# Performance work log

Measured on AMD Instinct MI355X. Metric: run time of the kernel, lower is better.

Reference implementation:

```python
import jax, jax.numpy as jnp
import numpy as np

N = 50000       # n_nodes
E = 800000      # n_edges
DIN = 64
DH = 64
DOUT = 64


def setup_inputs() -> dict:
    key = jax.random.key(0)
    k0, k1, k2, k3, k4 = jax.random.split(key, 5)
    x = jax.random.normal(k0, (N, DIN), dtype=jnp.float32)
    edge_index = jax.random.randint(k1, (2, E), 0, N, dtype=jnp.int32)
    # learnable per-edge weight (nn.Parameter); positive init keeps gcn_norm well-defined
    edge_weight = jax.random.uniform(k2, (E,), jnp.float32, 0.1, 1.0)
    W1 = jax.random.normal(k3, (DH, DIN), dtype=jnp.float32) * (1.0 / np.sqrt(DIN))
    b1 = jnp.zeros((DH,), jnp.float32)
    W2 = jax.random.normal(k4, (DOUT, DH), dtype=jnp.float32) * (1.0 / np.sqrt(DH))
    b2 = jnp.zeros((DOUT,), jnp.float32)
    return {"x": x, "edge_weight": edge_weight, "W1": W1, "b1": b1,
            "W2": W2, "b2": b2, "edge_index": edge_index}


def _gcn_norm(edge_index, edge_weight, n):
    # PyG gcn_norm: add self-loops (weight 1), symmetric normalization.
    loop = jnp.arange(n, dtype=edge_index.dtype)
    row = jnp.concatenate([edge_index[0], loop])   # source nodes
    col = jnp.concatenate([edge_index[1], loop])   # target nodes
    w = jnp.concatenate([edge_weight, jnp.ones((n,), edge_weight.dtype)])
    deg = jax.ops.segment_sum(w, col, num_segments=n)
    dinv = jnp.where(deg > 0, jax.lax.rsqrt(jnp.where(deg > 0, deg, 1.0)), 0.0)
    norm = dinv[row] * w * dinv[col]               # [E + N]
    return row, col, norm


def _gcn_layer(x, W, b, row, col, norm, n):
    h = x @ W.T                                     # [N, out]
    # gather source features, scale by norm, scatter-add into targets
    out = jax.ops.segment_sum(h[row] * norm[:, None], col, num_segments=n)
    return out + b


def reference(x, edge_weight, W1, b1, W2, b2, edge_index):
    n = x.shape[0]
    row, col, norm = _gcn_norm(edge_index, edge_weight, n)
    h = _gcn_layer(x, W1, b1, row, col, norm, n)
    h = jax.nn.relu(h)                              # self.pre: ReLU + Dropout (identity in eval)
    return _gcn_layer(h, W2, b2, row, col, norm, n)
```

## Files before the change

kernel.cpp:

```cpp
#include <hip/hip_runtime.h>

#define D 64
#define GN 128
#define SW 68
#define SX 132
#define MAXDEG 64
#define RBITS_C 8
#define RANGE_C 256
#define MAXB_C 5120
#define RANGE_F 64
#define APB 2048

typedef unsigned long long u64;
typedef unsigned int u32;
typedef unsigned short u16;
typedef unsigned char u8;

__device__ __forceinline__ float4 fma4(float4 w, float s, float4 c) {
    c.x = fmaf(w.x, s, c.x); c.y = fmaf(w.y, s, c.y);
    c.z = fmaf(w.z, s, c.z); c.w = fmaf(w.w, s, c.w);
    return c;
}

__device__ __forceinline__ u32 f2bf(float f) {
    u32 u = __float_as_uint(f);
    return (u + 0x7FFFu + ((u >> 16) & 1u)) >> 16;
}
__device__ __forceinline__ u32 pack2(float a, float b) { return f2bf(a) | (f2bf(b) << 16); }
__device__ __forceinline__ float blo(u32 u) { return __uint_as_float(u << 16); }
__device__ __forceinline__ float bhi(u32 u) { return __uint_as_float(u & 0xFFFF0000u); }

__global__ __launch_bounds__(256) void k_bucket(
        const int* __restrict__ ei, const float* __restrict__ ew,
        u64* __restrict__ barr, u32* __restrict__ gcount, int E, int NB) {
    __shared__ u64 srec[APB];
    __shared__ u8  sbkt[APB];
    __shared__ u32 scnt[256];
    __shared__ u32 sbase[256];

    int t = threadIdx.x;
    int e0 = blockIdx.x * APB;
    int ne = min(APB, E - e0);

    for (int i = t; i < 256; i += 256) scnt[i] = 0;
    __syncthreads();

    for (int i = t; i < ne; i += 256) {
        int e   = e0 + i;
        int r   = ei[e];
        int c   = ei[(size_t)E + e];
        float w = ew[e];
        int b   = c >> RBITS_C;
        srec[i] = ((u64)__float_as_uint(w) << 32)
                | (u32)r | ((u32)(c & (RANGE_C - 1)) << 20);
        sbkt[i] = (u8)b;
        atomicAdd(&scnt[b], 1u);
    }
    __syncthreads();

    for (int i = t; i < NB; i += 256) {
        u32 cnt = scnt[i];
        sbase[i] = cnt ? atomicAdd(&gcount[i], cnt) : 0u;
        scnt[i] = 0;
    }
    __syncthreads();

    for (int i = t; i < ne; i += 256) {
        int b   = sbkt[i];
        u32 rk  = atomicAdd(&scnt[b], 1u);
        u32 pos = sbase[b] + rk;
        if (pos < MAXB_C) barr[(size_t)b * MAXB_C + pos] = srec[i];
    }
}

__global__ __launch_bounds__(256) void k_csr(
        const u64* __restrict__ barr, const u32* __restrict__ gcount,
        u64* __restrict__ degcnt, int2* __restrict__ eg, int N) {
    __shared__ __align__(16) int2 seg[RANGE_F * MAXDEG];
    __shared__ u32   scnt[RANGE_F];
    __shared__ float sdeg[RANGE_F];

    int fb = blockIdx.x;
    int cb = fb >> 2;
    int sub = fb & 3;
    int t = threadIdx.x;
    u32 cnt = min(gcount[cb], (u32)MAXB_C);
    int base_c = fb << 6;

    if (t < RANGE_F) { scnt[t] = 0; sdeg[t] = 1.0f; }
    __syncthreads();

    const u64* bp = barr + (size_t)cb * MAXB_C;
    for (u32 i = t; i < cnt; i += 256) {
        u64 rec = bp[i];
        int cl8 = (int)((rec >> 20) & 0xFFu);
        if ((cl8 >> 6) != sub) continue;
        int cl  = cl8 & (RANGE_F - 1);
        int src = (int)(rec & 0xFFFFFu);
        u32 wb  = (u32)(rec >> 32);
        u32 rank = atomicAdd(&scnt[cl], 1u);
        atomicAdd(&sdeg[cl], __uint_as_float(wb));
        if (rank < MAXDEG) seg[(cl << 6) + rank] = make_int2(src, (int)wb);
    }
    __syncthreads();

    if (t < RANGE_F) {
        int n = base_c + t;
        if (n < N) {
            u32 c2 = min(scnt[t], (u32)MAXDEG);
            float dd = rsqrtf(sdeg[t]);
            degcnt[n] = ((u64)c2 << 32) | (u64)__float_as_uint(dd);
        }
    }

    int nt = min(RANGE_F, N - base_c);
    const int4* s4 = (const int4*)seg;
    int4* d4 = (int4*)(eg + ((size_t)base_c << 6));
    int tot = nt << 5;
    for (int i = t; i < tot; i += 256) {
        int cl = i >> 5;
        int lv = (int)min(scnt[cl], (u32)MAXDEG);
        if (((i & 31) << 1) < lv) d4[i] = s4[i];
    }
}

__global__ __launch_bounds__(256) void k_fold(
        const u64* __restrict__ degcnt, int2* __restrict__ eg, int N, int nwaves) {
    int lane = threadIdx.x & 63;
    int w0 = blockIdx.x * 4 + (threadIdx.x >> 6);
    const u32* dv = (const u32*)degcnt;

    for (int n = w0; n < N; n += nwaves) {
        u64 dcn = degcnt[n];
        int c = min((int)(dcn >> 32), MAXDEG);
        float dinv_n = __uint_as_float((u32)dcn);
        if (lane < c) {
            size_t s = ((size_t)n << 6) + lane;
            int2 ee = eg[s];
            float di = __uint_as_float(dv[(size_t)ee.x << 1]);
            float wf = __int_as_float(ee.y) * di * dinv_n;
            eg[s] = make_int2(ee.x, __float_as_int(wf));
        }
    }
}

__global__ __launch_bounds__(256) void k_gemm(
        const float* __restrict__ in, const float* __restrict__ W,
        u16* __restrict__ h, int N) {
    __shared__ __align__(16) float sWt[D * SW];
    __shared__ __align__(16) float sxT[D * SX];

    int t = threadIdx.x;
    int node0 = blockIdx.x * GN;

    for (int i = t; i < D * D / 4; i += 256) {
        int j = i >> 4, k4 = i & 15;
        float4 w = ((const float4*)W)[i];
        sWt[(4 * k4 + 0) * SW + j] = w.x;
        sWt[(4 * k4 + 1) * SW + j] = w.y;
        sWt[(4 * k4 + 2) * SW + j] = w.z;
        sWt[(4 * k4 + 3) * SW + j] = w.w;
    }
    for (int i = t; i < GN * D / 4; i += 256) {
        int nn = i >> 4, k4 = i & 15;
        int n = node0 + nn;
        float4 v = make_float4(0.f, 0.f, 0.f, 0.f);
        if (n < N) v = ((const float4*)(in + (size_t)n * D))[k4];
        sxT[(4 * k4 + 0) * SX + nn] = v.x;
        sxT[(4 * k4 + 1) * SX + nn] = v.y;
        sxT[(4 * k4 + 2) * SX + nn] = v.z;
        sxT[(4 * k4 + 3) * SX + nn] = v.w;
    }
    __syncthreads();

    int jg = (t & 7) * 8;
    int ng = (t >> 3) * 4;
    float4 a0[4], a1[4];
    #pragma unroll
    for (int a = 0; a < 4; ++a) {
        a0[a] = make_float4(0.f, 0.f, 0.f, 0.f);
        a1[a] = make_float4(0.f, 0.f, 0.f, 0.f);
    }

    #pragma unroll 8
    for (int k = 0; k < D; ++k) {
        const float* wr = &sWt[k * SW + jg];
        float4 w0 = *(const float4*)wr;
        float4 w1 = *(const float4*)(wr + 4);
        float4 xv = *(const float4*)&sxT[k * SX + ng];
        a0[0] = fma4(w0, xv.x, a0[0]);  a1[0] = fma4(w1, xv.x, a1[0]);
        a0[1] = fma4(w0, xv.y, a0[1]);  a1[1] = fma4(w1, xv.y, a1[1]);
        a0[2] = fma4(w0, xv.z, a0[2]);  a1[2] = fma4(w1, xv.z, a1[2]);
        a0[3] = fma4(w0, xv.w, a0[3]);  a1[3] = fma4(w1, xv.w, a1[3]);
    }

    #pragma unroll
    for (int a = 0; a < 4; ++a) {
        int n = node0 + ng + a;
        if (n >= N) continue;
        uint4 st;
        st.x = pack2(a0[a].x, a0[a].y);
        st.y = pack2(a0[a].z, a0[a].w);
        st.z = pack2(a1[a].x, a1[a].y);
        st.w = pack2(a1[a].z, a1[a].w);
        *(uint4*)(h + (size_t)n * D + jg) = st;
    }
}

__device__ __forceinline__ void gather8(
        const u16* __restrict__ h, const u64* __restrict__ degcnt,
        const int2* __restrict__ eg, float4 bia, float4 bib,
        u64* __restrict__ se,
        int n, int lane, float acc[8]) {
    int g = lane >> 3;
    int f = (lane & 7) * 8;
    u64 dcn = degcnt[n];
    int c = min((int)(dcn >> 32), MAXDEG);
    float dinv_n = __uint_as_float((u32)dcn);

    size_t s = (size_t)n << 6;
    if (lane < c) {
        int2 ee = eg[s + lane];
        se[lane] = ((u64)(u32)ee.y << 32) | (u32)ee.x;
    }

    #pragma unroll
    for (int i = 0; i < 8; ++i) acc[i] = 0.f;

    if (g == 0) {
        float d2 = dinv_n * dinv_n;
        uint4 hv = *(const uint4*)(h + ((size_t)n << 6) + f);
        acc[0] = fmaf(blo(hv.x), d2, bia.x); acc[1] = fmaf(bhi(hv.x), d2, bia.y);
        acc[2] = fmaf(blo(hv.y), d2, bia.z); acc[3] = fmaf(bhi(hv.y), d2, bia.w);
        acc[4] = fmaf(blo(hv.z), d2, bib.x); acc[5] = fmaf(bhi(hv.z), d2, bib.y);
        acc[6] = fmaf(blo(hv.w), d2, bib.z); acc[7] = fmaf(bhi(hv.w), d2, bib.w);
    }

    #pragma unroll
    for (int k = 0; k < 8; ++k) {
        int e = g + (k << 3);
        if (e < c) {
            u64 rec = se[e];
            int src = (int)(u32)rec;
            float w = __uint_as_float((u32)(rec >> 32));
            uint4 hv = *(const uint4*)(h + ((size_t)src << 6) + f);
            acc[0] = fmaf(blo(hv.x), w, acc[0]); acc[1] = fmaf(bhi(hv.x), w, acc[1]);
            acc[2] = fmaf(blo(hv.y), w, acc[2]); acc[3] = fmaf(bhi(hv.y), w, acc[3]);
            acc[4] = fmaf(blo(hv.z), w, acc[4]); acc[5] = fmaf(bhi(hv.z), w, acc[5]);
            acc[6] = fmaf(blo(hv.w), w, acc[6]); acc[7] = fmaf(bhi(hv.w), w, acc[7]);
        }
    }
}

__global__ __launch_bounds__(512) void k_agg_g2(
        const u16* __restrict__ h, const u64* __restrict__ degcnt,
        const int2* __restrict__ eg, const float* __restrict__ b1,
        const float* __restrict__ W2, u16* __restrict__ h2, int N) {
    __shared__ __align__(16) float4 sA[8 * 64];
    __shared__ __align__(16) float4 sB[8 * 64];
    __shared__ u64 sedge[8][64];

    int t = threadIdx.x;
    {
        int jj = t >> 6, l = t & 63;
        int gg = l >> 3, kk = l & 7;
        const float4* w4 = (const float4*)(W2 + ((size_t)(gg * 8 + jj) << 6) + kk * 8);
        sA[t] = w4[0];
        sB[t] = w4[1];
    }
    __syncthreads();

    int wid = t >> 6, lane = t & 63;
    int n = blockIdx.x * 8 + wid;
    if (n >= N) return;
    int g = lane >> 3, f = (lane & 7) * 8;

    float4 bia = *(const float4*)(b1 + f);
    float4 bib = *(const float4*)(b1 + f + 4);

    float acc[8];
    gather8(h, degcnt, eg, bia, bib, sedge[wid], n, lane, acc);

    #pragma unroll
    for (int k = 0; k < 8; ++k) {
        acc[k] += __shfl_xor(acc[k], 8);
        acc[k] += __shfl_xor(acc[k], 16);
        acc[k] += __shfl_xor(acc[k], 32);
    }

    float r[8];
    #pragma unroll
    for (int k = 0; k < 8; ++k) r[k] = fmaxf(acc[k], 0.f);

    float p[8];
    #pragma unroll
    for (int jj = 0; jj < 8; ++jj) {
        float4 wa = sA[(jj << 6) + lane];
        float4 wb = sB[(jj << 6) + lane];
        float v;
        v = r[0] * wa.x;         v = fmaf(r[1], wa.y, v);
        v = fmaf(r[2], wa.z, v); v = fmaf(r[3], wa.w, v);
        v = fmaf(r[4], wb.x, v); v = fmaf(r[5], wb.y, v);
        v = fmaf(r[6], wb.z, v); v = fmaf(r[7], wb.w, v);
        p[jj] = v;
    }
    #pragma unroll
    for (int jj = 0; jj < 8; ++jj) {
        p[jj] += __shfl_xor(p[jj], 1);
        p[jj] += __shfl_xor(p[jj], 2);
        p[jj] += __shfl_xor(p[jj], 4);
    }

    if ((lane & 7) == 0) {
        uint4 st;
        st.x = pack2(p[0], p[1]);
        st.y = pack2(p[2], p[3]);
        st.z = pack2(p[4], p[5]);
        st.w = pack2(p[6], p[7]);
        *(uint4*)(h2 + ((size_t)n << 6) + g * 8) = st;
    }
}

__global__ __launch_bounds__(256) void k_aggregate(
        const u16* __restrict__ h, const u64* __restrict__ degcnt,
        const int2* __restrict__ eg, const float* __restrict__ b,
        float* __restrict__ out, int N) {
    __shared__ u64 sedge[4][64];

    int t = threadIdx.x, wid = t >> 6, lane = t & 63;
    int n = blockIdx.x * 4 + wid;
    if (n >= N) return;
    int g = lane >> 3, f = (lane & 7) * 8;

    float4 bia = *(const float4*)(b + f);
    float4 bib = *(const float4*)(b + f + 4);

    float acc[8];
    gather8(h, degcnt, eg, bia, bib, sedge[wid], n, lane, acc);

    #pragma unroll
    for (int k = 0; k < 8; ++k) {
        acc[k] += __shfl_xor(acc[k], 8);
        acc[k] += __shfl_xor(acc[k], 16);
        acc[k] += __shfl_xor(acc[k], 32);
    }

    if (g == 0) {
        float4* o = (float4*)(out + ((size_t)n << 6) + f);
        o[0] = make_float4(acc[0], acc[1], acc[2], acc[3]);
        o[1] = make_float4(acc[4], acc[5], acc[6], acc[7]);
    }
}

extern "C" void kernel_launch(void* const* d_in, const int* in_sizes, int n_in,
                              void* d_out, int out_size, void* d_ws, size_t ws_size,
                              hipStream_t stream) {
    const float* x  = (const float*)d_in[0];
    const float* ew = (const float*)d_in[1];
    const float* W1 = (const float*)d_in[2];
    const float* b1 = (const float*)d_in[3];
    const float* W2 = (const float*)d_in[4];
    const float* b2 = (const float*)d_in[5];
    const int*   ei = (const int*)d_in[6];

    int N = in_sizes[0] / D;
    int E = in_sizes[1];
    int NBC = (N + RANGE_C - 1) >> RBITS_C;
    int NBF = (N + RANGE_F - 1) / RANGE_F;
    float* out = (float*)d_out;

    char* p = (char*)d_ws;
    u64*   degcnt = (u64*)p;   p += (size_t)N * 8;
    int2*  eg     = (int2*)p;  p += (size_t)N * MAXDEG * 8;
    u16*   h      = (u16*)p;   p += (size_t)N * D * 2;
    u16*   h2     = (u16*)p;   p += (size_t)N * D * 2;
    u64*   barr   = (u64*)p;   p += (size_t)NBC * MAXB_C * 8;
    u32*   gcount = (u32*)p;   p += 4096;

    dim3 blk(256);
    int gemm_grid   = (N + GN - 1) / GN;
    int bucket_grid = (E + APB - 1) / APB;
    int fold_grid   = 3125;
    int aggf_grid   = (N + 7) / 8;
    int agg_grid    = (N + 3) / 4;

    hipMemsetAsync(gcount, 0, 4096, stream);

    k_bucket<<<dim3(bucket_grid), blk, 0, stream>>>(ei, ew, barr, gcount, E, NBC);
    k_csr<<<dim3(NBF), blk, 0, stream>>>(barr, gcount, degcnt, eg, N);
    k_fold<<<dim3(fold_grid), blk, 0, stream>>>(degcnt, eg, N, fold_grid * 4);

    k_gemm<<<dim3(gemm_grid), blk, 0, stream>>>(x, W1, h, N);

    k_agg_g2<<<dim3(aggf_grid), dim3(512), 0, stream>>>(h, degcnt, eg, b1, W2, h2, N);

    k_aggregate<<<dim3(agg_grid), blk, 0, stream>>>(h2, degcnt, eg, b2, out, N);
}
```

Measured before the change: 193.4 us.

## Fuse edge-weight normalization into first aggregation and use one-feature-per-lane gathers

```diff
diff --git a/kernel.cpp b/kernel.cpp
--- a/kernel.cpp
+++ b/kernel.cpp
@@ -27,8 +27,7 @@
     return (u + 0x7FFFu + ((u >> 16) & 1u)) >> 16;
 }
 __device__ __forceinline__ u32 pack2(float a, float b) { return f2bf(a) | (f2bf(b) << 16); }
-__device__ __forceinline__ float blo(u32 u) { return __uint_as_float(u << 16); }
-__device__ __forceinline__ float bhi(u32 u) { return __uint_as_float(u & 0xFFFF0000u); }
+__device__ __forceinline__ float bf2f(u32 hv) { return __uint_as_float(hv << 16); }
 
 __global__ __launch_bounds__(256) void k_bucket(
         const int* __restrict__ ei, const float* __restrict__ ew,
@@ -124,26 +123,6 @@
     }
 }
 
-__global__ __launch_bounds__(256) void k_fold(
-        const u64* __restrict__ degcnt, int2* __restrict__ eg, int N, int nwaves) {
-    int lane = threadIdx.x & 63;
-    int w0 = blockIdx.x * 4 + (threadIdx.x >> 6);
-    const u32* dv = (const u32*)degcnt;
-
-    for (int n = w0; n < N; n += nwaves) {
-        u64 dcn = degcnt[n];
-        int c = min((int)(dcn >> 32), MAXDEG);
-        float dinv_n = __uint_as_float((u32)dcn);
-        if (lane < c) {
-            size_t s = ((size_t)n << 6) + lane;
-            int2 ee = eg[s];
-            float di = __uint_as_float(dv[(size_t)ee.x << 1]);
-            float wf = __int_as_float(ee.y) * di * dinv_n;
-            eg[s] = make_int2(ee.x, __float_as_int(wf));
-        }
-    }
-}
-
 __global__ __launch_bounds__(256) void k_gemm(
         const float* __restrict__ in, const float* __restrict__ W,
         u16* __restrict__ h, int N) {
@@ -207,58 +186,14 @@
     }
 }
 
-__device__ __forceinline__ void gather8(
-        const u16* __restrict__ h, const u64* __restrict__ degcnt,
-        const int2* __restrict__ eg, float4 bia, float4 bib,
-        u64* __restrict__ se,
-        int n, int lane, float acc[8]) {
-    int g = lane >> 3;
-    int f = (lane & 7) * 8;
-    u64 dcn = degcnt[n];
-    int c = min((int)(dcn >> 32), MAXDEG);
-    float dinv_n = __uint_as_float((u32)dcn);
-
-    size_t s = (size_t)n << 6;
-    if (lane < c) {
-        int2 ee = eg[s + lane];
-        se[lane] = ((u64)(u32)ee.y << 32) | (u32)ee.x;
-    }
-
-    #pragma unroll
-    for (int i = 0; i < 8; ++i) acc[i] = 0.f;
-
-    if (g == 0) {
-        float d2 = dinv_n * dinv_n;
-        uint4 hv = *(const uint4*)(h + ((size_t)n << 6) + f);
-        acc[0] = fmaf(blo(hv.x), d2, bia.x); acc[1] = fmaf(bhi(hv.x), d2, bia.y);
-        acc[2] = fmaf(blo(hv.y), d2, bia.z); acc[3] = fmaf(bhi(hv.y), d2, bia.w);
-        acc[4] = fmaf(blo(hv.z), d2, bib.x); acc[5] = fmaf(bhi(hv.z), d2, bib.y);
-        acc[6] = fmaf(blo(hv.w), d2, bib.z); acc[7] = fmaf(bhi(hv.w), d2, bib.w);
-    }
-
-    #pragma unroll
-    for (int k = 0; k < 8; ++k) {
-        int e = g + (k << 3);
-        if (e < c) {
-            u64 rec = se[e];
-            int src = (int)(u32)rec;
-            float w = __uint_as_float((u32)(rec >> 32));
-            uint4 hv = *(const uint4*)(h + ((size_t)src << 6) + f);
-            acc[0] = fmaf(blo(hv.x), w, acc[0]); acc[1] = fmaf(bhi(hv.x), w, acc[1]);
-            acc[2] = fmaf(blo(hv.y), w, acc[2]); acc[3] = fmaf(bhi(hv.y), w, acc[3]);
-            acc[4] = fmaf(blo(hv.z), w, acc[4]); acc[5] = fmaf(bhi(hv.z), w, acc[5]);
-            acc[6] = fmaf(blo(hv.w), w, acc[6]); acc[7] = fmaf(bhi(hv.w), w, acc[7]);
-        }
-    }
-}
-
 __global__ __launch_bounds__(512) void k_agg_g2(
         const u16* __restrict__ h, const u64* __restrict__ degcnt,
-        const int2* __restrict__ eg, const float* __restrict__ b1,
+        int2* __restrict__ eg, const float* __restrict__ b1,
         const float* __restrict__ W2, u16* __restrict__ h2, int N) {
     __shared__ __align__(16) float4 sA[8 * 64];
     __shared__ __align__(16) float4 sB[8 * 64];
     __shared__ u64 sedge[8][64];
+    __shared__ __align__(16) float srow[8][64];
 
     int t = threadIdx.x;
     {
@@ -273,24 +208,41 @@
     int wid = t >> 6, lane = t & 63;
     int n = blockIdx.x * 8 + wid;
     if (n >= N) return;
-    int g = lane >> 3, f = (lane & 7) * 8;
-
-    float4 bia = *(const float4*)(b1 + f);
-    float4 bib = *(const float4*)(b1 + f + 4);
-
-    float acc[8];
-    gather8(h, degcnt, eg, bia, bib, sedge[wid], n, lane, acc);
-
-    #pragma unroll
-    for (int k = 0; k < 8; ++k) {
-        acc[k] += __shfl_xor(acc[k], 8);
-        acc[k] += __shfl_xor(acc[k], 16);
-        acc[k] += __shfl_xor(acc[k], 32);
-    }
-
-    float r[8];
-    #pragma unroll
-    for (int k = 0; k < 8; ++k) r[k] = fmaxf(acc[k], 0.f);
+
+    const u32* dv = (const u32*)degcnt;
+    u64 dcn = degcnt[n];
+    int c = min((int)(dcn >> 32), MAXDEG);
+    float dinv_n = __uint_as_float((u32)dcn);
+    u64* se = sedge[wid];
+    size_t s = (size_t)n << 6;
+
+    if (lane < c) {
+        int2 ee = eg[s + lane];
+        float di = __uint_as_float(dv[(size_t)ee.x << 1]);
+        float wf = __int_as_float(ee.y) * di * dinv_n;
+        eg[s + lane] = make_int2(ee.x, __float_as_int(wf));
+        se[lane] = ((u64)__float_as_uint(wf) << 32) | (u32)ee.x;
+    }
+
+    float acc = b1[lane];
+    acc = fmaf(bf2f(h[s + lane]), dinv_n * dinv_n, acc);
+
+    #pragma unroll
+    for (int e = 0; e < MAXDEG; ++e) {
+        if (e < c) {
+            u64 rec = se[e];
+            u32 src = (u32)rec;
+            float wf = __uint_as_float((u32)(rec >> 32));
+            acc = fmaf(bf2f(h[((size_t)src << 6) + lane]), wf, acc);
+        }
+    }
+
+    float r = fmaxf(acc, 0.f);
+    srow[wid][lane] = r;
+
+    int g = lane >> 3, kb = (lane & 7) * 8;
+    float4 ra = *(const float4*)&srow[wid][kb];
+    float4 rb = *(const float4*)&srow[wid][kb + 4];
 
     float p[8];
     #pragma unroll
@@ -298,10 +250,10 @@
         float4 wa = sA[(jj << 6) + lane];
         float4 wb = sB[(jj << 6) + lane];
         float v;
-        v = r[0] * wa.x;         v = fmaf(r[1], wa.y, v);
-        v = fmaf(r[2], wa.z, v); v = fmaf(r[3], wa.w, v);
-        v = fmaf(r[4], wb.x, v); v = fmaf(r[5], wb.y, v);
-        v = fmaf(r[6], wb.z, v); v = fmaf(r[7], wb.w, v);
+        v = ra.x * wa.x;         v = fmaf(ra.y, wa.y, v);
+        v = fmaf(ra.z, wa.z, v); v = fmaf(ra.w, wa.w, v);
+        v = fmaf(rb.x, wb.x, v); v = fmaf(rb.y, wb.y, v);
+        v = fmaf(rb.z, wb.z, v); v = fmaf(rb.w, wb.w, v);
         p[jj] = v;
     }
     #pragma unroll
@@ -317,7 +269,7 @@
         st.y = pack2(p[2], p[3]);
         st.z = pack2(p[4], p[5]);
         st.w = pack2(p[6], p[7]);
-        *(uint4*)(h2 + ((size_t)n << 6) + g * 8) = st;
+        *(uint4*)(h2 + s + g * 8) = st;
     }
 }
 
@@ -330,26 +282,32 @@
     int t = threadIdx.x, wid = t >> 6, lane = t & 63;
     int n = blockIdx.x * 4 + wid;
     if (n >= N) return;
-    int g = lane >> 3, f = (lane & 7) * 8;
-
-    float4 bia = *(const float4*)(b + f);
-    float4 bib = *(const float4*)(b + f + 4);
-
-    float acc[8];
-    gather8(h, degcnt, eg, bia, bib, sedge[wid], n, lane, acc);
-
-    #pragma unroll
-    for (int k = 0; k < 8; ++k) {
-        acc[k] += __shfl_xor(acc[k], 8);
-        acc[k] += __shfl_xor(acc[k], 16);
-        acc[k] += __shfl_xor(acc[k], 32);
-    }
-
-    if (g == 0) {
-        float4* o = (float4*)(out + ((size_t)n << 6) + f);
-        o[0] = make_float4(acc[0], acc[1], acc[2], acc[3]);
-        o[1] = make_float4(acc[4], acc[5], acc[6], acc[7]);
-    }
+
+    u64 dcn = degcnt[n];
+    int c = min((int)(dcn >> 32), MAXDEG);
+    float dinv_n = __uint_as_float((u32)dcn);
+    u64* se = sedge[wid];
+    size_t s = (size_t)n << 6;
+
+    if (lane < c) {
+        int2 ee = eg[s + lane];
+        se[lane] = ((u64)(u32)ee.y << 32) | (u32)ee.x;
+    }
+
+    float acc = b[lane];
+    acc = fmaf(bf2f(h[s + lane]), dinv_n * dinv_n, acc);
+
+    #pragma unroll
+    for (int e = 0; e < MAXDEG; ++e) {
+        if (e < c) {
+            u64 rec = se[e];
+            u32 src = (u32)rec;
+            float wf = __uint_as_float((u32)(rec >> 32));
+            acc = fmaf(bf2f(h[((size_t)src << 6) + lane]), wf, acc);
+        }
+    }
+
+    out[s + lane] = acc;
 }
 
 extern "C" void kernel_launch(void* const* d_in, const int* in_sizes, int n_in,
@@ -380,7 +338,6 @@
     dim3 blk(256);
     int gemm_grid   = (N + GN - 1) / GN;
     int bucket_grid = (E + APB - 1) / APB;
-    int fold_grid   = 3125;
     int aggf_grid   = (N + 7) / 8;
     int agg_grid    = (N + 3) / 4;
 
@@ -388,7 +345,6 @@
 
     k_bucket<<<dim3(bucket_grid), blk, 0, stream>>>(ei, ew, barr, gcount, E, NBC);
     k_csr<<<dim3(NBF), blk, 0, stream>>>(barr, gcount, degcnt, eg, N);
-    k_fold<<<dim3(fold_grid), blk, 0, stream>>>(degcnt, eg, N, fold_grid * 4);
 
     k_gemm<<<dim3(gemm_grid), blk, 0, stream>>>(x, W1, h, N);
 
```

Result: slower. 247.7 us (+28.1%).

## Fold edge normalization into first aggregation and reorder second layer as aggregate-then-GEMM

Applied to the files above, without the earlier changes.

```diff
diff --git a/kernel.cpp b/kernel.cpp
--- a/kernel.cpp
+++ b/kernel.cpp
@@ -124,26 +124,6 @@
     }
 }
 
-__global__ __launch_bounds__(256) void k_fold(
-        const u64* __restrict__ degcnt, int2* __restrict__ eg, int N, int nwaves) {
-    int lane = threadIdx.x & 63;
-    int w0 = blockIdx.x * 4 + (threadIdx.x >> 6);
-    const u32* dv = (const u32*)degcnt;
-
-    for (int n = w0; n < N; n += nwaves) {
-        u64 dcn = degcnt[n];
-        int c = min((int)(dcn >> 32), MAXDEG);
-        float dinv_n = __uint_as_float((u32)dcn);
-        if (lane < c) {
-            size_t s = ((size_t)n << 6) + lane;
-            int2 ee = eg[s];
-            float di = __uint_as_float(dv[(size_t)ee.x << 1]);
-            float wf = __int_as_float(ee.y) * di * dinv_n;
-            eg[s] = make_int2(ee.x, __float_as_int(wf));
-        }
-    }
-}
-
 __global__ __launch_bounds__(256) void k_gemm(
         const float* __restrict__ in, const float* __restrict__ W,
         u16* __restrict__ h, int N) {
@@ -207,13 +187,73 @@
     }
 }
 
+__global__ __launch_bounds__(256) void k_gemmb(
+        const float* __restrict__ in, const float* __restrict__ W,
+        const float* __restrict__ bias, float* __restrict__ out, int N) {
+    __shared__ __align__(16) float sWt[D * SW];
+    __shared__ __align__(16) float sxT[D * SX];
+
+    int t = threadIdx.x;
+    int node0 = blockIdx.x * GN;
+
+    for (int i = t; i < D * D / 4; i += 256) {
+        int j = i >> 4, k4 = i & 15;
+        float4 w = ((const float4*)W)[i];
+        sWt[(4 * k4 + 0) * SW + j] = w.x;
+        sWt[(4 * k4 + 1) * SW + j] = w.y;
+        sWt[(4 * k4 + 2) * SW + j] = w.z;
+        sWt[(4 * k4 + 3) * SW + j] = w.w;
+    }
+    for (int i = t; i < GN * D / 4; i += 256) {
+        int nn = i >> 4, k4 = i & 15;
+        int n = node0 + nn;
+        float4 v = make_float4(0.f, 0.f, 0.f, 0.f);
+        if (n < N) v = ((const float4*)(in + (size_t)n * D))[k4];
+        sxT[(4 * k4 + 0) * SX + nn] = v.x;
+        sxT[(4 * k4 + 1) * SX + nn] = v.y;
+        sxT[(4 * k4 + 2) * SX + nn] = v.z;
+        sxT[(4 * k4 + 3) * SX + nn] = v.w;
+    }
+    __syncthreads();
+
+    int jg = (t & 7) * 8;
+    int ng = (t >> 3) * 4;
+    float4 bb0 = *(const float4*)(bias + jg);
+    float4 bb1 = *(const float4*)(bias + jg + 4);
+    float4 a0[4], a1[4];
+    #pragma unroll
+    for (int a = 0; a < 4; ++a) { a0[a] = bb0; a1[a] = bb1; }
+
+    #pragma unroll 8
+    for (int k = 0; k < D; ++k) {
+        const float* wr = &sWt[k * SW + jg];
+        float4 w0 = *(const float4*)wr;
+        float4 w1 = *(const float4*)(wr + 4);
+        float4 xv = *(const float4*)&sxT[k * SX + ng];
+        a0[0] = fma4(w0, xv.x, a0[0]);  a1[0] = fma4(w1, xv.x, a1[0]);
+        a0[1] = fma4(w0, xv.y, a0[1]);  a1[1] = fma4(w1, xv.y, a1[1]);
+        a0[2] = fma4(w0, xv.z, a0[2]);  a1[2] = fma4(w1, xv.z, a1[2]);
+        a0[3] = fma4(w0, xv.w, a0[3]);  a1[3] = fma4(w1, xv.w, a1[3]);
+    }
+
+    #pragma unroll
+    for (int a = 0; a < 4; ++a) {
+        int n = node0 + ng + a;
+        if (n >= N) continue;
+        float* o = out + (size_t)n * D + jg;
+        *(float4*)o       = a0[a];
+        *(float4*)(o + 4) = a1[a];
+    }
+}
+
+template<bool FOLD>
 __device__ __forceinline__ void gather8(
         const u16* __restrict__ h, const u64* __restrict__ degcnt,
-        const int2* __restrict__ eg, float4 bia, float4 bib,
-        u64* __restrict__ se,
-        int n, int lane, float acc[8]) {
+        int2* __restrict__ eg, float4 bia, float4 bib,
+        u64* __restrict__ se, int n, int lane, float acc[8]) {
     int g = lane >> 3;
     int f = (lane & 7) * 8;
+    const u32* dv = (const u32*)degcnt;
     u64 dcn = degcnt[n];
     int c = min((int)(dcn >> 32), MAXDEG);
     float dinv_n = __uint_as_float((u32)dcn);
@@ -221,7 +261,15 @@
     size_t s = (size_t)n << 6;
     if (lane < c) {
         int2 ee = eg[s + lane];
-        se[lane] = ((u64)(u32)ee.y << 32) | (u32)ee.x;
+        float wf;
+        if (FOLD) {
+            wf = __int_as_float(ee.y);
+        } else {
+            float di = __uint_as_float(dv[(size_t)ee.x << 1]);
+            wf = __int_as_float(ee.y) * di * dinv_n;
+            eg[s + lane] = make_int2(ee.x, __float_as_int(wf));
+        }
+        se[lane] = ((u64)__float_as_uint(wf) << 32) | (u32)ee.x;
     }
 
     #pragma unroll
@@ -229,7 +277,7 @@
 
     if (g == 0) {
         float d2 = dinv_n * dinv_n;
-        uint4 hv = *(const uint4*)(h + ((size_t)n << 6) + f);
+        uint4 hv = *(const uint4*)(h + s + f);
         acc[0] = fmaf(blo(hv.x), d2, bia.x); acc[1] = fmaf(bhi(hv.x), d2, bia.y);
         acc[2] = fmaf(blo(hv.y), d2, bia.z); acc[3] = fmaf(bhi(hv.y), d2, bia.w);
         acc[4] = fmaf(blo(hv.z), d2, bib.x); acc[5] = fmaf(bhi(hv.z), d2, bib.y);
@@ -252,26 +300,14 @@
     }
 }
 
-__global__ __launch_bounds__(512) void k_agg_g2(
+__global__ __launch_bounds__(256) void k_agg_relu(
         const u16* __restrict__ h, const u64* __restrict__ degcnt,
-        const int2* __restrict__ eg, const float* __restrict__ b1,
-        const float* __restrict__ W2, u16* __restrict__ h2, int N) {
-    __shared__ __align__(16) float4 sA[8 * 64];
-    __shared__ __align__(16) float4 sB[8 * 64];
-    __shared__ u64 sedge[8][64];
-
-    int t = threadIdx.x;
-    {
-        int jj = t >> 6, l = t & 63;
-        int gg = l >> 3, kk = l & 7;
-        const float4* w4 = (const float4*)(W2 + ((size_t)(gg * 8 + jj) << 6) + kk * 8);
-        sA[t] = w4[0];
-        sB[t] = w4[1];
-    }
-    __syncthreads();
-
-    int wid = t >> 6, lane = t & 63;
-    int n = blockIdx.x * 8 + wid;
+        int2* __restrict__ eg, const float* __restrict__ b1,
+        u16* __restrict__ h2, int N) {
+    __shared__ u64 sedge[4][64];
+
+    int t = threadIdx.x, wid = t >> 6, lane = t & 63;
+    int n = blockIdx.x * 4 + wid;
     if (n >= N) return;
     int g = lane >> 3, f = (lane & 7) * 8;
 
@@ -279,7 +315,7 @@
     float4 bib = *(const float4*)(b1 + f + 4);
 
     float acc[8];
-    gather8(h, degcnt, eg, bia, bib, sedge[wid], n, lane, acc);
+    gather8<false>(h, degcnt, eg, bia, bib, sedge[wid], n, lane, acc);
 
     #pragma unroll
     for (int k = 0; k < 8; ++k) {
@@ -288,43 +324,19 @@
         acc[k] += __shfl_xor(acc[k], 32);
     }
 
-    float r[8];
-    #pragma unroll
-    for (int k = 0; k < 8; ++k) r[k] = fmaxf(acc[k], 0.f);
-
-    float p[8];
-    #pragma unroll
-    for (int jj = 0; jj < 8; ++jj) {
-        float4 wa = sA[(jj << 6) + lane];
-        float4 wb = sB[(jj << 6) + lane];
-        float v;
-        v = r[0] * wa.x;         v = fmaf(r[1], wa.y, v);
-        v = fmaf(r[2], wa.z, v); v = fmaf(r[3], wa.w, v);
-        v = fmaf(r[4], wb.x, v); v = fmaf(r[5], wb.y, v);
-        v = fmaf(r[6], wb.z, v); v = fmaf(r[7], wb.w, v);
-        p[jj] = v;
-    }
-    #pragma unroll
-    for (int jj = 0; jj < 8; ++jj) {
-        p[jj] += __shfl_xor(p[jj], 1);
-        p[jj] += __shfl_xor(p[jj], 2);
-        p[jj] += __shfl_xor(p[jj], 4);
-    }
-
-    if ((lane & 7) == 0) {
+    if (g == 0) {
         uint4 st;
-        st.x = pack2(p[0], p[1]);
-        st.y = pack2(p[2], p[3]);
-        st.z = pack2(p[4], p[5]);
-        st.w = pack2(p[6], p[7]);
-        *(uint4*)(h2 + ((size_t)n << 6) + g * 8) = st;
+        st.x = pack2(fmaxf(acc[0], 0.f), fmaxf(acc[1], 0.f));
+        st.y = pack2(fmaxf(acc[2], 0.f), fmaxf(acc[3], 0.f));
+        st.z = pack2(fmaxf(acc[4], 0.f), fmaxf(acc[5], 0.f));
+        st.w = pack2(fmaxf(acc[6], 0.f), fmaxf(acc[7], 0.f));
+        *(uint4*)(h2 + ((size_t)n << 6) + f) = st;
     }
 }
 
 __global__ __launch_bounds__(256) void k_aggregate(
         const u16* __restrict__ h, const u64* __restrict__ degcnt,
-        const int2* __restrict__ eg, const float* __restrict__ b,
-        float* __restrict__ out, int N) {
+        int2* __restrict__ eg, float* __restrict__ z, int N) {
     __shared__ u64 sedge[4][64];
 
     int t = threadIdx.x, wid = t >> 6, lane = t & 63;
@@ -332,11 +344,9 @@
     if (n >= N) return;
     int g = lane >> 3, f = (lane & 7) * 8;
 
-    float4 bia = *(const float4*)(b + f);
-    float4 bib = *(const float4*)(b + f + 4);
-
+    float4 zz = make_float4(0.f, 0.f, 0.f, 0.f);
     float acc[8];
-    gather8(h, degcnt, eg, bia, bib, sedge[wid], n, lane, acc);
+    gather8<true>(h, degcnt, eg, zz, zz, sedge[wid], n, lane, acc);
 
     #pragma unroll
     for (int k = 0; k < 8; ++k) {
@@ -346,7 +356,7 @@
     }
 
     if (g == 0) {
-        float4* o = (float4*)(out + ((size_t)n << 6) + f);
+        float4* o = (float4*)(z + ((size_t)n << 6) + f);
         o[0] = make_float4(acc[0], acc[1], acc[2], acc[3]);
         o[1] = make_float4(acc[4], acc[5], acc[6], acc[7]);
     }
@@ -374,25 +384,24 @@
     int2*  eg     = (int2*)p;  p += (size_t)N * MAXDEG * 8;
     u16*   h      = (u16*)p;   p += (size_t)N * D * 2;
     u16*   h2     = (u16*)p;   p += (size_t)N * D * 2;
+    float* z      = (float*)p; p += (size_t)N * D * 4;
     u64*   barr   = (u64*)p;   p += (size_t)NBC * MAXB_C * 8;
     u32*   gcount = (u32*)p;   p += 4096;
 
     dim3 blk(256);
     int gemm_grid   = (N + GN - 1) / GN;
     int bucket_grid = (E + APB - 1) / APB;
-    int fold_grid   = 3125;
-    int aggf_grid   = (N + 7) / 8;
     int agg_grid    = (N + 3) / 4;
 
     hipMemsetAsync(gcount, 0, 4096, stream);
 
     k_bucket<<<dim3(bucket_grid), blk, 0, stream>>>(ei, ew, barr, gcount, E, NBC);
     k_csr<<<dim3(NBF), blk, 0, stream>>>(barr, gcount, degcnt, eg, N);
-    k_fold<<<dim3(fold_grid), blk, 0, stream>>>(degcnt, eg, N, fold_grid * 4);
 
     k_gemm<<<dim3(gemm_grid), blk, 0, stream>>>(x, W1, h, N);
 
-    k_agg_g2<<<dim3(aggf_grid), dim3(512), 0, stream>>>(h, degcnt, eg, b1, W2, h2, N);
-
-    k_aggregate<<<dim3(agg_grid), blk, 0, stream>>>(h2, degcnt, eg, b2, out, N);
-}
+    k_agg_relu<<<dim3(agg_grid), blk, 0, stream>>>(h, degcnt, eg, b1, h2, N);
+
+    k_aggregate<<<dim3(agg_grid), blk, 0, stream>>>(h2, degcnt, eg, z, N);
+    k_gemmb<<<dim3(gemm_grid), blk, 0, stream>>>(z, W2, b2, out, N);
+}
```

Measured after the change: 182.1 us. 1.06x faster.
